# Kernel optimization log

Hardware: AMD Instinct MI355X
Metric: run time of the kernel (lower is better)

Reference implementation:

```python
import jax, jax.numpy as jnp
import numpy as np
from jax import lax

K, INC, OUC = 6, 64, 32
H, W = 512, 512
WIN = 128  # min(128, min(H,W)) for training path
ITERATION = 2  # torch uses random.randint(1,3); fixed for determinism


def setup_inputs() -> dict:
    key = jax.random.key(0)
    ks = jax.random.split(key, 12)
    s = 0.05
    return {
        "x": jax.random.uniform(ks[0], (K, 3, H, W), jnp.float32),
        "pred_list": jax.random.uniform(ks[1], (K, 3, H, W), jnp.float32),
        "feat_list": jax.random.normal(ks[2], (K, INC, H, W), jnp.float32) * 0.1,
        "split_w": jax.random.normal(ks[3], (3 * OUC, INC, 3, 3), jnp.float32) * s,
        "split_b": jax.random.normal(ks[4], (3 * OUC,), jnp.float32) * s,
        "merge1_w": jax.random.normal(ks[5], (INC, 3 * OUC + 3, 3, 3), jnp.float32) * s,
        "merge1_b": jax.random.normal(ks[6], (INC,), jnp.float32) * s,
        "merge2_w": jax.random.normal(ks[7], (INC, INC, 3, 3), jnp.float32) * s,
        "merge2_b": jax.random.normal(ks[8], (INC,), jnp.float32) * s,
        "head_w": jax.random.normal(ks[9], (3, INC, 3, 3), jnp.float32) * s,
        "head_b": jax.random.normal(ks[10], (3,), jnp.float32) * s,
    }


def _conv(x, w, b, groups=1):
    y = lax.conv_general_dilated(
        x, w, (1, 1), ((1, 1), (1, 1)),
        dimension_numbers=("NCHW", "OIHW", "NCHW"), feature_group_count=groups)
    return y + b[None, :, None, None]


def _get_box(pred_list):
    # B_cat = mean of bg channel, T_cat = sum of fg channel; distance map [H,W]
    B_cat = pred_list[:, 2].mean(axis=0)
    T_cat = pred_list[:, 0].sum(axis=0)
    distance = jnp.abs(1.0 - T_cat - B_cat)
    # nearest-neighbor downsample by 0.1: out[i,j] = in[10*i, 10*j]
    hs, ws = H // 10, W // 10
    ds = distance[::10, ::10][:hs, :ws]
    # NMS keep[0] (training path uses boxes[0:1]) == global argmax of score
    idx = jnp.argmax(ds.reshape(-1))
    cx = (idx % ws) * 10
    cy = (idx // ws) * 10
    half = WIN // 2
    x1, y1 = cx - half, cy - half
    x2, y2 = cx + half, cy + half
    ox = (-jnp.minimum(x1, 0) + jnp.minimum(W - x1, 0)
          - jnp.minimum(x2, 0) + jnp.minimum(W - x2, 0))
    oy = (-jnp.minimum(y1, 0) + jnp.minimum(H - y1, 0)
          - jnp.minimum(y2, 0) + jnp.minimum(H - y2, 0))
    return (y1 + oy).astype(jnp.int32), (x1 + ox).astype(jnp.int32)


def reference(x, pred_list, feat_list, split_w, split_b,
              merge1_w, merge1_b, merge2_w, merge2_b, head_w, head_b):
    c = INC
    y1, x1 = _get_box(pred_list)  # box fixed across iterations (computed once)
    x_patch = lax.dynamic_slice(x, (0, 0, y1, x1), (K, 3, WIN, WIN))
    feat_patch = lax.dynamic_slice(feat_list, (0, 0, y1, x1), (K, INC, WIN, WIN))
    feat_tiled = jnp.tile(feat_patch, (1, 3, 1, 1))
    denom = max(K - 1, 1)

    pl = pred_list
    for _ in range(ITERATION):
        pred_patch = lax.dynamic_slice(pl, (0, 0, y1, x1), (K, 3, WIN, WIN))
        # cat([p0.repeat(c), p1.repeat(c), p2.repeat(c)]) == repeat each channel c times
        attention = jnp.repeat(pred_patch, c, axis=1)
        fs = _conv(feat_tiled * attention, split_w, split_b, groups=3)
        f0, f1, f2 = fs[:, :OUC], fs[:, OUC:2 * OUC], fs[:, 2 * OUC:]
        feat_t = f1.sum(0, keepdims=True) / denom - f0.sum(0, keepdims=True) + 2.0 * f0
        feat_r = f0.sum(0, keepdims=True) - f0 + f1
        feat_b = jnp.broadcast_to(f2.mean(0, keepdims=True), f2.shape)
        fcat = jnp.concatenate([feat_t, feat_r, feat_b, x_patch], axis=1)
        h1 = jax.nn.leaky_relu(_conv(fcat, merge1_w, merge1_b), 0.2)
        fm = _conv(h1, merge2_w, merge2_b)
        pr = _conv(fm, head_w, head_b)
        inner = (jnp.tanh(pr[:, :, 10:WIN - 10, 10:WIN - 10]) + 1.0) / 2.0
        pl = lax.dynamic_update_slice(pl, inner, (0, 0, y1 + 10, x1 + 10))
    return pl
```

## Files before the change

### kernel.cpp

```cpp
#include <hip/hip_runtime.h>
#include <math.h>

typedef __attribute__((ext_vector_type(8))) short short8_t;
typedef __attribute__((ext_vector_type(4))) float f32x4;

#define Hh 512
#define Ww 512
#define IMG (Hh * Ww)
#define WINP 128
#define PP (WINP * WINP)

__device__ __forceinline__ unsigned short f2bf(float f) {
    unsigned int u = __builtin_bit_cast(unsigned int, f);
    u += 0x7fffu + ((u >> 16) & 1u);
    return (unsigned short)(u >> 16);
}
__device__ __forceinline__ float bf2f(unsigned short h) {
    unsigned int u = ((unsigned int)h) << 16;
    return __builtin_bit_cast(float, u);
}

__global__ void box_kernel(const float* __restrict__ pred, int* __restrict__ box) {
    int tid = threadIdx.x;
    float best = -1.0f; int bidx = 0x7fffffff;
    for (int cand = tid; cand < 51 * 51; cand += 256) {
        int i = cand / 51, j = cand % 51;
        int y = i * 10, x = j * 10;
        float T = 0.f, Bv = 0.f;
#pragma unroll
        for (int k = 0; k < 6; ++k) {
            T  += pred[((k * 3 + 0) * Hh + y) * Ww + x];
            Bv += pred[((k * 3 + 2) * Hh + y) * Ww + x];
        }
        float d = fabsf(1.0f - T - Bv / 6.0f);
        if (d > best || (d == best && cand < bidx)) { best = d; bidx = cand; }
    }
    __shared__ float sv[256];
    __shared__ int   si[256];
    sv[tid] = best; si[tid] = bidx;
    __syncthreads();
    for (int s = 128; s > 0; s >>= 1) {
        if (tid < s) {
            if (sv[tid + s] > sv[tid] || (sv[tid + s] == sv[tid] && si[tid + s] < si[tid])) {
                sv[tid] = sv[tid + s]; si[tid] = si[tid + s];
            }
        }
        __syncthreads();
    }
    if (tid == 0) {
        int idx = si[0];
        int cy = (idx / 51) * 10, cx = (idx % 51) * 10;
        int yy = cy - 64; yy = yy < 0 ? 0 : (yy > Hh - WINP ? Hh - WINP : yy);
        int xx = cx - 64; xx = xx < 0 ? 0 : (xx > Ww - WINP ? Ww - WINP : xx);
        box[0] = yy; box[1] = xx;
    }
}

__global__ void copy_kernel(const float4* __restrict__ src, float4* __restrict__ dst) {
    int i = blockIdx.x * 256 + threadIdx.x;
    dst[i] = src[i];
}

__global__ void prep_weights(const float* __restrict__ sw, const float* __restrict__ m1w,
                             const float* __restrict__ m2w, const float* __restrict__ hw,
                             unsigned short* __restrict__ WF)
{
    int idx = blockIdx.x * 256 + threadIdx.x;
    int j = idx & 7;
    int lane = (idx >> 3) & 63;
    int frag = idx >> 9;
    int n16 = lane & 15;
    int ko = (lane >> 4) * 8 + j;
    float v = 0.f;
    if (frag < 108) {
        int g = frag / 36; int r = frag % 36; int kc = r / 18; r %= 18; int tap = r / 2; int nf = r & 1;
        int oc = g * 32 + nf * 16 + n16; int ic = kc * 32 + ko;
        v = sw[(oc * 64 + ic) * 9 + tap];
    } else if (frag < 252) {
        int r = frag - 108; int half = r / 72; r %= 72; int kc = r / 18; r %= 18; int tap = r / 2; int nf = r & 1;
        int oc = half * 32 + nf * 16 + n16; int ic = kc * 32 + ko;
        if (ic < 99) v = m1w[(oc * 99 + ic) * 9 + tap];
    } else if (frag < 324) {
        int r = frag - 252; int half = r / 36; r %= 36; int kc = r / 18; r %= 18; int tap = r / 2; int nf = r & 1;
        int oc = half * 32 + nf * 16 + n16; int ic = kc * 32 + ko;
        v = m2w[(oc * 64 + ic) * 9 + tap];
    } else {
        int r = frag - 324; int kc = r / 9; int tap = r % 9;
        int ic = kc * 32 + ko;
        if (n16 < 3) v = hw[(n16 * 64 + ic) * 9 + tap];
    }
    WF[idx] = f2bf(v);
}

__global__ void prep_featcl(const float* __restrict__ feat, const int* __restrict__ box,
                            unsigned short* __restrict__ featcl)
{
    int row = blockIdx.x;
    int k = blockIdx.y;
    int t = threadIdx.x;
    int y1 = box[0], x1 = box[1];
    __shared__ unsigned short s[128 * 64];
    for (int i = 0; i < 32; ++i) {
        int idx = t + i * 256;
        int ic = idx >> 7, c = idx & 127;
        s[c * 64 + ic] = f2bf(feat[((size_t)(k * 64 + ic) * Hh + y1 + row) * Ww + x1 + c]);
    }
    __syncthreads();
    if (t < 128) {
        unsigned short* dst = &featcl[((size_t)k * 16384 + row * 128 + t) * 64];
        for (int i = 0; i < 8; ++i)
            *(short8_t*)&dst[i * 8] = *(short8_t*)&s[t * 64 + i * 8];
    }
}

__global__ __launch_bounds__(256) void split_mfma(
    const unsigned short* __restrict__ featcl, const float* __restrict__ pl,
    const unsigned short* __restrict__ WF, const float* __restrict__ sb,
    const int* __restrict__ box, unsigned short* __restrict__ fscl)
{
    const int tid = threadIdx.x;
    const int l = tid & 63, w = tid >> 6;
    const int T = blockIdx.x;
    const int k = blockIdx.y / 3, g = blockIdx.y % 3;
    const int ty0 = (T >> 3) * 16, tx0 = (T & 7) * 16;
    const int y1 = box[0], x1 = box[1];

    __shared__ __align__(16) unsigned short s_a[10368];
    __shared__ __align__(16) unsigned short s_b[9216];

    f32x4 acc[4][2];
#pragma unroll
    for (int mf = 0; mf < 4; ++mf)
#pragma unroll
        for (int nf = 0; nf < 2; ++nf) acc[mf][nf] = (f32x4){0.f, 0.f, 0.f, 0.f};

    const float* plg = pl + (size_t)(k * 3 + g) * IMG + (size_t)y1 * Ww + x1;
    const unsigned short* fck = featcl + (size_t)k * 16384 * 64;

    for (int kc = 0; kc < 2; ++kc) {
        __syncthreads();
#pragma unroll
        for (int i = 0; i < 6; ++i) {
            int s = tid + i * 256;
            if (s < 1296) {
                int pxs = s >> 2, q = s & 3;
                int r = pxs / 18, c = pxs - r * 18;
                int py = ty0 - 1 + r, px = tx0 - 1 + c;
                short8_t o;
                if (py >= 0 && py < WINP && px >= 0 && px < WINP) {
                    float pv = plg[py * Ww + px];
                    short8_t f = *(const short8_t*)&fck[(size_t)(py * WINP + px) * 64 + kc * 32 + q * 8];
#pragma unroll
                    for (int e = 0; e < 8; ++e) o[e] = (short)f2bf(bf2f((unsigned short)f[e]) * pv);
                } else {
#pragma unroll
                    for (int e = 0; e < 8; ++e) o[e] = 0;
                }
                *(short8_t*)&s_a[(r * 18 + c) * 32 + q * 8] = o;
            }
        }
        {
            const unsigned short* src = WF + (size_t)((g * 2 + kc) * 18) * 512;
#pragma unroll
            for (int i = 0; i < 5; ++i) {
                int cch = tid + i * 256;
                if (cch < 1152)
                    *(short8_t*)&s_b[cch * 8] = *(const short8_t*)&src[cch * 8];
            }
        }
        __syncthreads();
#pragma unroll
        for (int tap = 0; tap < 9; ++tap) {
            int dy = tap / 3, dx = tap % 3;
            short8_t a[4];
#pragma unroll
            for (int mf = 0; mf < 4; ++mf)
                a[mf] = *(const short8_t*)&s_a[((w * 4 + mf + dy) * 18 + (l & 15) + dx) * 32 + (l >> 4) * 8];
#pragma unroll
            for (int nf = 0; nf < 2; ++nf) {
                short8_t bfr = *(const short8_t*)&s_b[((tap * 2 + nf) * 64 + l) * 8];
#pragma unroll
                for (int mf = 0; mf < 4; ++mf)
                    acc[mf][nf] = __builtin_amdgcn_mfma_f32_16x16x32_bf16(a[mf], bfr, acc[mf][nf], 0, 0, 0);
            }
        }
    }
    __syncthreads();
    unsigned short* s_t = s_a;
#pragma unroll
    for (int nf = 0; nf < 2; ++nf) {
        float bias = sb[g * 32 + nf * 16 + (l & 15)];
#pragma unroll
        for (int mf = 0; mf < 4; ++mf) {
            int row = w * 4 + mf;
#pragma unroll
            for (int r = 0; r < 4; ++r) {
                int col = (l >> 4) * 4 + r;
                s_t[(row * 16 + col) * 32 + nf * 16 + (l & 15)] = f2bf(acc[mf][nf][r] + bias);
            }
        }
    }
    __syncthreads();
    {
        int row = tid >> 4, col = tid & 15;
        size_t gpx = (size_t)(ty0 + row) * WINP + tx0 + col;
        unsigned short* dst = fscl + ((size_t)k * 16384 + gpx) * 96 + g * 32;
#pragma unroll
        for (int i = 0; i < 4; ++i)
            *(short8_t*)&dst[i * 8] = *(short8_t*)&s_t[tid * 32 + i * 8];
    }
}

__global__ void reduce_kernel(const unsigned short* __restrict__ fscl, float* __restrict__ Scl)
{
    int tg = blockIdx.x * 256 + threadIdx.x;
    int px = tg >> 2, q = tg & 3;
    float s0[8], s1[8], s2[8];
#pragma unroll
    for (int e = 0; e < 8; ++e) { s0[e] = 0.f; s1[e] = 0.f; s2[e] = 0.f; }
#pragma unroll
    for (int k = 0; k < 6; ++k) {
        const unsigned short* p = &fscl[((size_t)k * 16384 + px) * 96 + q * 8];
        short8_t a0 = *(const short8_t*)&p[0];
        short8_t a1 = *(const short8_t*)&p[32];
        short8_t a2 = *(const short8_t*)&p[64];
#pragma unroll
        for (int e = 0; e < 8; ++e) {
            s0[e] += bf2f((unsigned short)a0[e]);
            s1[e] += bf2f((unsigned short)a1[e]);
            s2[e] += bf2f((unsigned short)a2[e]);
        }
    }
    float* d = &Scl[(size_t)px * 96 + q * 8];
#pragma unroll
    for (int e = 0; e < 8; ++e) {
        d[e]      = s1[e] * 0.2f - s0[e];
        d[32 + e] = s0[e];
        d[64 + e] = s2[e] * (1.f / 6.f);
    }
}

__global__ __launch_bounds__(256) void merge1_mfma(
    const unsigned short* __restrict__ fscl, const float* __restrict__ Scl,
    const float* __restrict__ x, const unsigned short* __restrict__ WF,
    const float* __restrict__ m1b, const int* __restrict__ box,
    unsigned short* __restrict__ h1cl)
{
    const int tid = threadIdx.x;
    const int l = tid & 63, w = tid >> 6;
    const int T = blockIdx.x;
    const int k = blockIdx.y >> 1, half = blockIdx.y & 1;
    const int ty0 = (T >> 3) * 16, tx0 = (T & 7) * 16;
    const int y1 = box[0], x1 = box[1];

    __shared__ __align__(16) unsigned short s_a[10368];
    __shared__ __align__(16) unsigned short s_b[9216];

    f32x4 acc[4][2];
#pragma unroll
    for (int mf = 0; mf < 4; ++mf)
#pragma unroll
        for (int nf = 0; nf < 2; ++nf) acc[mf][nf] = (f32x4){0.f, 0.f, 0.f, 0.f};

    for (int kc = 0; kc < 4; ++kc) {
        __syncthreads();
#pragma unroll
        for (int i = 0; i < 6; ++i) {
            int s = tid + i * 256;
            if (s < 1296) {
                int pxs = s >> 2, q = s & 3;
                int r = pxs / 18, c = pxs - r * 18;
                int py = ty0 - 1 + r, px = tx0 - 1 + c;
                short8_t o;
#pragma unroll
                for (int e = 0; e < 8; ++e) o[e] = 0;
                if (py >= 0 && py < WINP && px >= 0 && px < WINP) {
                    size_t gpx = (size_t)py * WINP + px;
                    if (kc == 0) {
                        short8_t f0 = *(const short8_t*)&fscl[((size_t)k * 16384 + gpx) * 96 + q * 8];
                        const float* S = &Scl[gpx * 96 + q * 8];
#pragma unroll
                        for (int e = 0; e < 8; ++e)
                            o[e] = (short)f2bf(S[e] + 2.f * bf2f((unsigned short)f0[e]));
                    } else if (kc == 1) {
                        const unsigned short* fp = &fscl[((size_t)k * 16384 + gpx) * 96];
                        short8_t f0 = *(const short8_t*)&fp[q * 8];
                        short8_t f1 = *(const short8_t*)&fp[32 + q * 8];
                        const float* S = &Scl[gpx * 96 + 32 + q * 8];
#pragma unroll
                        for (int e = 0; e < 8; ++e)
                            o[e] = (short)f2bf(S[e] - bf2f((unsigned short)f0[e]) + bf2f((unsigned short)f1[e]));
                    } else if (kc == 2) {
                        const float* S = &Scl[gpx * 96 + 64 + q * 8];
#pragma unroll
                        for (int e = 0; e < 8; ++e) o[e] = (short)f2bf(S[e]);
                    } else {
                        if (q == 0) {
#pragma unroll
                            for (int ch = 0; ch < 3; ++ch)
                                o[ch] = (short)f2bf(x[(size_t)(k * 3 + ch) * IMG + (size_t)(y1 + py) * Ww + x1 + px]);
                        }
                    }
                }
                *(short8_t*)&s_a[(r * 18 + c) * 32 + q * 8] = o;
            }
        }
        {
            const unsigned short* src = WF + (size_t)(108 + (half * 4 + kc) * 18) * 512;
#pragma unroll
            for (int i = 0; i < 5; ++i) {
                int cch = tid + i * 256;
                if (cch < 1152)
                    *(short8_t*)&s_b[cch * 8] = *(const short8_t*)&src[cch * 8];
            }
        }
        __syncthreads();
#pragma unroll
        for (int tap = 0; tap < 9; ++tap) {
            int dy = tap / 3, dx = tap % 3;
            short8_t a[4];
#pragma unroll
            for (int mf = 0; mf < 4; ++mf)
                a[mf] = *(const short8_t*)&s_a[((w * 4 + mf + dy) * 18 + (l & 15) + dx) * 32 + (l >> 4) * 8];
#pragma unroll
            for (int nf = 0; nf < 2; ++nf) {
                short8_t bfr = *(const short8_t*)&s_b[((tap * 2 + nf) * 64 + l) * 8];
#pragma unroll
                for (int mf = 0; mf < 4; ++mf)
                    acc[mf][nf] = __builtin_amdgcn_mfma_f32_16x16x32_bf16(a[mf], bfr, acc[mf][nf], 0, 0, 0);
            }
        }
    }
    __syncthreads();
    unsigned short* s_t = s_a;
#pragma unroll
    for (int nf = 0; nf < 2; ++nf) {
        float bias = m1b[half * 32 + nf * 16 + (l & 15)];
#pragma unroll
        for (int mf = 0; mf < 4; ++mf) {
            int row = w * 4 + mf;
#pragma unroll
            for (int r = 0; r < 4; ++r) {
                int col = (l >> 4) * 4 + r;
                float v = acc[mf][nf][r] + bias;
                v = v >= 0.f ? v : 0.2f * v;
                s_t[(row * 16 + col) * 32 + nf * 16 + (l & 15)] = f2bf(v);
            }
        }
    }
    __syncthreads();
    {
        int row = tid >> 4, col = tid & 15;
        size_t gpx = (size_t)(ty0 + row) * WINP + tx0 + col;
        unsigned short* dst = h1cl + ((size_t)k * 16384 + gpx) * 64 + half * 32;
#pragma unroll
        for (int i = 0; i < 4; ++i)
            *(short8_t*)&dst[i * 8] = *(short8_t*)&s_t[tid * 32 + i * 8];
    }
}

__global__ __launch_bounds__(256) void merge2_mfma(
    const unsigned short* __restrict__ h1cl, const unsigned short* __restrict__ WF,
    const float* __restrict__ m2b, unsigned short* __restrict__ h2cl)
{
    const int tid = threadIdx.x;
    const int l = tid & 63, w = tid >> 6;
    const int T = blockIdx.x;
    const int k = blockIdx.y >> 1, half = blockIdx.y & 1;
    const int ty0 = (T >> 3) * 16, tx0 = (T & 7) * 16;

    __shared__ __align__(16) unsigned short s_a[10368];
    __shared__ __align__(16) unsigned short s_b[9216];

    f32x4 acc[4][2];
#pragma unroll
    for (int mf = 0; mf < 4; ++mf)
#pragma unroll
        for (int nf = 0; nf < 2; ++nf) acc[mf][nf] = (f32x4){0.f, 0.f, 0.f, 0.f};

    const unsigned short* ink = h1cl + (size_t)k * 16384 * 64;

    for (int kc = 0; kc < 2; ++kc) {
        __syncthreads();
#pragma unroll
        for (int i = 0; i < 6; ++i) {
            int s = tid + i * 256;
            if (s < 1296) {
                int pxs = s >> 2, q = s & 3;
                int r = pxs / 18, c = pxs - r * 18;
                int py = ty0 - 1 + r, px = tx0 - 1 + c;
                short8_t o;
                if (py >= 0 && py < WINP && px >= 0 && px < WINP) {
                    o = *(const short8_t*)&ink[(size_t)(py * WINP + px) * 64 + kc * 32 + q * 8];
                } else {
#pragma unroll
                    for (int e = 0; e < 8; ++e) o[e] = 0;
                }
                *(short8_t*)&s_a[(r * 18 + c) * 32 + q * 8] = o;
            }
        }
        {
            const unsigned short* src = WF + (size_t)(252 + (half * 2 + kc) * 18) * 512;
#pragma unroll
            for (int i = 0; i < 5; ++i) {
                int cch = tid + i * 256;
                if (cch < 1152)
                    *(short8_t*)&s_b[cch * 8] = *(const short8_t*)&src[cch * 8];
            }
        }
        __syncthreads();
#pragma unroll
        for (int tap = 0; tap < 9; ++tap) {
            int dy = tap / 3, dx = tap % 3;
            short8_t a[4];
#pragma unroll
            for (int mf = 0; mf < 4; ++mf)
                a[mf] = *(const short8_t*)&s_a[((w * 4 + mf + dy) * 18 + (l & 15) + dx) * 32 + (l >> 4) * 8];
#pragma unroll
            for (int nf = 0; nf < 2; ++nf) {
                short8_t bfr = *(const short8_t*)&s_b[((tap * 2 + nf) * 64 + l) * 8];
#pragma unroll
                for (int mf = 0; mf < 4; ++mf)
                    acc[mf][nf] = __builtin_amdgcn_mfma_f32_16x16x32_bf16(a[mf], bfr, acc[mf][nf], 0, 0, 0);
            }
        }
    }
    __syncthreads();
    unsigned short* s_t = s_a;
#pragma unroll
    for (int nf = 0; nf < 2; ++nf) {
        float bias = m2b[half * 32 + nf * 16 + (l & 15)];
#pragma unroll
        for (int mf = 0; mf < 4; ++mf) {
            int row = w * 4 + mf;
#pragma unroll
            for (int r = 0; r < 4; ++r) {
                int col = (l >> 4) * 4 + r;
                s_t[(row * 16 + col) * 32 + nf * 16 + (l & 15)] = f2bf(acc[mf][nf][r] + bias);
            }
        }
    }
    __syncthreads();
    {
        int row = tid >> 4, col = tid & 15;
        size_t gpx = (size_t)(ty0 + row) * WINP + tx0 + col;
        unsigned short* dst = h2cl + ((size_t)k * 16384 + gpx) * 64 + half * 32;
#pragma unroll
        for (int i = 0; i < 4; ++i)
            *(short8_t*)&dst[i * 8] = *(short8_t*)&s_t[tid * 32 + i * 8];
    }
}

__global__ __launch_bounds__(256) void head_mfma(
    const unsigned short* __restrict__ h2cl, const unsigned short* __restrict__ WF,
    const float* __restrict__ hb, const int* __restrict__ box,
    float* __restrict__ out)
{
    const int tid = threadIdx.x;
    const int l = tid & 63, w = tid >> 6;
    const int T = blockIdx.x;
    const int k = blockIdx.y;
    const int oy0 = 10 + (T / 7) * 16, ox0 = 10 + (T % 7) * 16;
    const int y1 = box[0], x1 = box[1];

    __shared__ __align__(16) unsigned short s_a[10368];
    __shared__ __align__(16) unsigned short s_b[4608];

    f32x4 acc[4];
#pragma unroll
    for (int mf = 0; mf < 4; ++mf) acc[mf] = (f32x4){0.f, 0.f, 0.f, 0.f};

    const unsigned short* ink = h2cl + (size_t)k * 16384 * 64;

    for (int kc = 0; kc < 2; ++kc) {
        __syncthreads();
#pragma unroll
        for (int i = 0; i < 6; ++i) {
            int s = tid + i * 256;
            if (s < 1296) {
                int pxs = s >> 2, q = s & 3;
                int r = pxs / 18, c = pxs - r * 18;
                int py = oy0 - 1 + r, px = ox0 - 1 + c;
                *(short8_t*)&s_a[(r * 18 + c) * 32 + q * 8] =
                    *(const short8_t*)&ink[(size_t)(py * WINP + px) * 64 + kc * 32 + q * 8];
            }
        }
        {
            const unsigned short* src = WF + (size_t)(324 + kc * 9) * 512;
#pragma unroll
            for (int i = 0; i < 3; ++i) {
                int cch = tid + i * 256;
                if (cch < 576)
                    *(short8_t*)&s_b[cch * 8] = *(const short8_t*)&src[cch * 8];
            }
        }
        __syncthreads();
#pragma unroll
        for (int tap = 0; tap < 9; ++tap) {
            int dy = tap / 3, dx = tap % 3;
            short8_t bfr = *(const short8_t*)&s_b[(tap * 64 + l) * 8];
#pragma unroll
            for (int mf = 0; mf < 4; ++mf) {
                short8_t a = *(const short8_t*)&s_a[((w * 4 + mf + dy) * 18 + (l & 15) + dx) * 32 + (l >> 4) * 8];
                acc[mf] = __builtin_amdgcn_mfma_f32_16x16x32_bf16(a, bfr, acc[mf], 0, 0, 0);
            }
        }
    }
    int oc = l & 15;
    if (oc < 3) {
        float bias = hb[oc];
#pragma unroll
        for (int mf = 0; mf < 4; ++mf) {
            int row = oy0 + w * 4 + mf;
            if (row < 118) {
#pragma unroll
                for (int r = 0; r < 4; ++r) {
                    int col = ox0 + (l >> 4) * 4 + r;
                    if (col < 118) {
                        float v = (tanhf(acc[mf][r] + bias) + 1.0f) * 0.5f;
                        out[(size_t)(k * 3 + oc) * IMG + (size_t)(y1 + row) * Ww + x1 + col] = v;
                    }
                }
            }
        }
    }
}

extern "C" void kernel_launch(void* const* d_in, const int* in_sizes, int n_in,
                              void* d_out, int out_size, void* d_ws, size_t ws_size,
                              hipStream_t stream)
{
    const float* x       = (const float*)d_in[0];
    const float* pred    = (const float*)d_in[1];
    const float* feat    = (const float*)d_in[2];
    const float* split_w = (const float*)d_in[3];
    const float* split_b = (const float*)d_in[4];
    const float* m1w     = (const float*)d_in[5];
    const float* m1b     = (const float*)d_in[6];
    const float* m2w     = (const float*)d_in[7];
    const float* m2b     = (const float*)d_in[8];
    const float* hw      = (const float*)d_in[9];
    const float* hb      = (const float*)d_in[10];
    float* out = (float*)d_out;

    char* base = (char*)d_ws;
    size_t o = 0;
    int* box = (int*)(base + o);                  o += 256;
    unsigned short* WF = (unsigned short*)(base + o);      o += (size_t)175104 * 2;  o = (o + 255) & ~(size_t)255;
    unsigned short* featcl = (unsigned short*)(base + o);  o += (size_t)6 * 16384 * 64 * 2;
    unsigned short* fscl = (unsigned short*)(base + o);    o += (size_t)6 * 16384 * 96 * 2;
    float* Scl = (float*)(base + o);                       o += (size_t)16384 * 96 * 4;
    unsigned short* h1cl = (unsigned short*)(base + o);    o += (size_t)6 * 16384 * 64 * 2;
    unsigned short* h2cl = (unsigned short*)(base + o);    o += (size_t)6 * 16384 * 64 * 2;

    box_kernel<<<1, 256, 0, stream>>>(pred, box);
    prep_weights<<<684, 256, 0, stream>>>(split_w, m1w, m2w, hw, WF);
    prep_featcl<<<dim3(128, 6), 256, 0, stream>>>(feat, box, featcl);
    copy_kernel<<<4608, 256, 0, stream>>>((const float4*)pred, (float4*)out);

    for (int it = 0; it < 2; ++it) {
        split_mfma<<<dim3(64, 18), 256, 0, stream>>>(featcl, out, WF, split_b, box, fscl);
        reduce_kernel<<<256, 256, 0, stream>>>(fscl, Scl);
        merge1_mfma<<<dim3(64, 12), 256, 0, stream>>>(fscl, Scl, x, WF, m1b, box, h1cl);
        merge2_mfma<<<dim3(64, 12), 256, 0, stream>>>(h1cl, WF, m2b, h2cl);
        head_mfma<<<dim3(49, 6), 256, 0, stream>>>(h2cl, WF, hb, box, out);
    }
}
```

Before: 695.6 us.

## Read conv weights directly from global, reorder LDS layout, merge output-channel halves

All four conv kernels stop staging weights in shared memory and read the B fragments straight from global (L1/L2-cached) memory. The A-tile LDS layout changes from pixel-major to quarter-channel-major, which spreads lanes across banks. merge1 and merge2 now compute all 64 output channels per block instead of splitting them into halves, so the halo input tile is staged once. The cost is half as many blocks, more accumulator registers, and weight loads exposed to global latency inside the MFMA loop.

Result: slower. 805.3 us (+15.8%).

```diff
diff --git a/kernel.cpp b/kernel.cpp
--- a/kernel.cpp
+++ b/kernel.cpp
@@ -126,7 +126,6 @@
     const int y1 = box[0], x1 = box[1];
 
     __shared__ __align__(16) unsigned short s_a[10368];
-    __shared__ __align__(16) unsigned short s_b[9216];
 
     f32x4 acc[4][2];
 #pragma unroll
@@ -156,29 +155,21 @@
 #pragma unroll
                     for (int e = 0; e < 8; ++e) o[e] = 0;
                 }
-                *(short8_t*)&s_a[(r * 18 + c) * 32 + q * 8] = o;
-            }
-        }
-        {
-            const unsigned short* src = WF + (size_t)((g * 2 + kc) * 18) * 512;
-#pragma unroll
-            for (int i = 0; i < 5; ++i) {
-                int cch = tid + i * 256;
-                if (cch < 1152)
-                    *(short8_t*)&s_b[cch * 8] = *(const short8_t*)&src[cch * 8];
-            }
-        }
-        __syncthreads();
+                *(short8_t*)&s_a[(q * 324 + pxs) * 8] = o;
+            }
+        }
+        __syncthreads();
+        const unsigned short* Bp = WF + ((size_t)(g * 2 + kc) * 18) * 512 + (size_t)l * 8;
 #pragma unroll
         for (int tap = 0; tap < 9; ++tap) {
             int dy = tap / 3, dx = tap % 3;
             short8_t a[4];
 #pragma unroll
             for (int mf = 0; mf < 4; ++mf)
-                a[mf] = *(const short8_t*)&s_a[((w * 4 + mf + dy) * 18 + (l & 15) + dx) * 32 + (l >> 4) * 8];
+                a[mf] = *(const short8_t*)&s_a[((l >> 4) * 324 + (w * 4 + mf + dy) * 18 + (l & 15) + dx) * 8];
 #pragma unroll
             for (int nf = 0; nf < 2; ++nf) {
-                short8_t bfr = *(const short8_t*)&s_b[((tap * 2 + nf) * 64 + l) * 8];
+                short8_t bfr = *(const short8_t*)&Bp[(size_t)(tap * 2 + nf) * 512];
 #pragma unroll
                 for (int mf = 0; mf < 4; ++mf)
                     acc[mf][nf] = __builtin_amdgcn_mfma_f32_16x16x32_bf16(a[mf], bfr, acc[mf][nf], 0, 0, 0);
@@ -190,13 +181,14 @@
 #pragma unroll
     for (int nf = 0; nf < 2; ++nf) {
         float bias = sb[g * 32 + nf * 16 + (l & 15)];
+        int slot = nf * 2 + ((l & 15) >> 3);
 #pragma unroll
         for (int mf = 0; mf < 4; ++mf) {
             int row = w * 4 + mf;
 #pragma unroll
             for (int r = 0; r < 4; ++r) {
                 int col = (l >> 4) * 4 + r;
-                s_t[(row * 16 + col) * 32 + nf * 16 + (l & 15)] = f2bf(acc[mf][nf][r] + bias);
+                s_t[(slot * 256 + row * 16 + col) * 8 + (l & 7)] = f2bf(acc[mf][nf][r] + bias);
             }
         }
     }
@@ -207,7 +199,7 @@
         unsigned short* dst = fscl + ((size_t)k * 16384 + gpx) * 96 + g * 32;
 #pragma unroll
         for (int i = 0; i < 4; ++i)
-            *(short8_t*)&dst[i * 8] = *(short8_t*)&s_t[tid * 32 + i * 8];
+            *(short8_t*)&dst[i * 8] = *(short8_t*)&s_t[(i * 256 + tid) * 8];
     }
 }
 
@@ -249,18 +241,17 @@
     const int tid = threadIdx.x;
     const int l = tid & 63, w = tid >> 6;
     const int T = blockIdx.x;
-    const int k = blockIdx.y >> 1, half = blockIdx.y & 1;
+    const int k = blockIdx.y;
     const int ty0 = (T >> 3) * 16, tx0 = (T & 7) * 16;
     const int y1 = box[0], x1 = box[1];
 
     __shared__ __align__(16) unsigned short s_a[10368];
-    __shared__ __align__(16) unsigned short s_b[9216];
-
-    f32x4 acc[4][2];
+
+    f32x4 acc[4][4];
 #pragma unroll
     for (int mf = 0; mf < 4; ++mf)
 #pragma unroll
-        for (int nf = 0; nf < 2; ++nf) acc[mf][nf] = (f32x4){0.f, 0.f, 0.f, 0.f};
+        for (int n = 0; n < 4; ++n) acc[mf][n] = (f32x4){0.f, 0.f, 0.f, 0.f};
 
     for (int kc = 0; kc < 4; ++kc) {
         __syncthreads();
@@ -302,60 +293,59 @@
                         }
                     }
                 }
-                *(short8_t*)&s_a[(r * 18 + c) * 32 + q * 8] = o;
-            }
-        }
-        {
-            const unsigned short* src = WF + (size_t)(108 + (half * 4 + kc) * 18) * 512;
-#pragma unroll
-            for (int i = 0; i < 5; ++i) {
-                int cch = tid + i * 256;
-                if (cch < 1152)
-                    *(short8_t*)&s_b[cch * 8] = *(const short8_t*)&src[cch * 8];
-            }
-        }
-        __syncthreads();
+                *(short8_t*)&s_a[(q * 324 + pxs) * 8] = o;
+            }
+        }
+        __syncthreads();
+        const unsigned short* Bp = WF + ((size_t)(108 + kc * 18)) * 512 + (size_t)l * 8;
 #pragma unroll
         for (int tap = 0; tap < 9; ++tap) {
             int dy = tap / 3, dx = tap % 3;
             short8_t a[4];
 #pragma unroll
             for (int mf = 0; mf < 4; ++mf)
-                a[mf] = *(const short8_t*)&s_a[((w * 4 + mf + dy) * 18 + (l & 15) + dx) * 32 + (l >> 4) * 8];
-#pragma unroll
-            for (int nf = 0; nf < 2; ++nf) {
-                short8_t bfr = *(const short8_t*)&s_b[((tap * 2 + nf) * 64 + l) * 8];
+                a[mf] = *(const short8_t*)&s_a[((l >> 4) * 324 + (w * 4 + mf + dy) * 18 + (l & 15) + dx) * 8];
+#pragma unroll
+            for (int n = 0; n < 4; ++n) {
+                int half = n >> 1, nf2 = n & 1;
+                short8_t bfr = *(const short8_t*)&Bp[((size_t)half * 72 + tap * 2 + nf2) * 512];
 #pragma unroll
                 for (int mf = 0; mf < 4; ++mf)
-                    acc[mf][nf] = __builtin_amdgcn_mfma_f32_16x16x32_bf16(a[mf], bfr, acc[mf][nf], 0, 0, 0);
+                    acc[mf][n] = __builtin_amdgcn_mfma_f32_16x16x32_bf16(a[mf], bfr, acc[mf][n], 0, 0, 0);
             }
         }
     }
     __syncthreads();
     unsigned short* s_t = s_a;
 #pragma unroll
-    for (int nf = 0; nf < 2; ++nf) {
-        float bias = m1b[half * 32 + nf * 16 + (l & 15)];
-#pragma unroll
-        for (int mf = 0; mf < 4; ++mf) {
-            int row = w * 4 + mf;
-#pragma unroll
-            for (int r = 0; r < 4; ++r) {
-                int col = (l >> 4) * 4 + r;
-                float v = acc[mf][nf][r] + bias;
-                v = v >= 0.f ? v : 0.2f * v;
-                s_t[(row * 16 + col) * 32 + nf * 16 + (l & 15)] = f2bf(v);
-            }
-        }
-    }
-    __syncthreads();
-    {
-        int row = tid >> 4, col = tid & 15;
-        size_t gpx = (size_t)(ty0 + row) * WINP + tx0 + col;
-        unsigned short* dst = h1cl + ((size_t)k * 16384 + gpx) * 64 + half * 32;
-#pragma unroll
-        for (int i = 0; i < 4; ++i)
-            *(short8_t*)&dst[i * 8] = *(short8_t*)&s_t[tid * 32 + i * 8];
+    for (int h = 0; h < 2; ++h) {
+#pragma unroll
+        for (int nf2 = 0; nf2 < 2; ++nf2) {
+            int n = h * 2 + nf2;
+            float bias = m1b[n * 16 + (l & 15)];
+            int slot = nf2 * 2 + ((l & 15) >> 3);
+#pragma unroll
+            for (int mf = 0; mf < 4; ++mf) {
+                int row = w * 4 + mf;
+#pragma unroll
+                for (int r = 0; r < 4; ++r) {
+                    int col = (l >> 4) * 4 + r;
+                    float v = acc[mf][n][r] + bias;
+                    v = v >= 0.f ? v : 0.2f * v;
+                    s_t[(slot * 256 + row * 16 + col) * 8 + (l & 7)] = f2bf(v);
+                }
+            }
+        }
+        __syncthreads();
+        {
+            int row = tid >> 4, col = tid & 15;
+            size_t gpx = (size_t)(ty0 + row) * WINP + tx0 + col;
+            unsigned short* dst = h1cl + ((size_t)k * 16384 + gpx) * 64 + h * 32;
+#pragma unroll
+            for (int i = 0; i < 4; ++i)
+                *(short8_t*)&dst[i * 8] = *(short8_t*)&s_t[(i * 256 + tid) * 8];
+        }
+        __syncthreads();
     }
 }
 
@@ -366,17 +356,16 @@
     const int tid = threadIdx.x;
     const int l = tid & 63, w = tid >> 6;
     const int T = blockIdx.x;
-    const int k = blockIdx.y >> 1, half = blockIdx.y & 1;
+    const int k = blockIdx.y;
     const int ty0 = (T >> 3) * 16, tx0 = (T & 7) * 16;
 
     __shared__ __align__(16) unsigned short s_a[10368];
-    __shared__ __align__(16) unsigned short s_b[9216];
-
-    f32x4 acc[4][2];
+
+    f32x4 acc[4][4];
 #pragma unroll
     for (int mf = 0; mf < 4; ++mf)
 #pragma unroll
-        for (int nf = 0; nf < 2; ++nf) acc[mf][nf] = (f32x4){0.f, 0.f, 0.f, 0.f};
+        for (int n = 0; n < 4; ++n) acc[mf][n] = (f32x4){0.f, 0.f, 0.f, 0.f};
 
     const unsigned short* ink = h1cl + (size_t)k * 16384 * 64;
 
@@ -396,58 +385,57 @@
 #pragma unroll
                     for (int e = 0; e < 8; ++e) o[e] = 0;
                 }
-                *(short8_t*)&s_a[(r * 18 + c) * 32 + q * 8] = o;
-            }
-        }
-        {
-            const unsigned short* src = WF + (size_t)(252 + (half * 2 + kc) * 18) * 512;
-#pragma unroll
-            for (int i = 0; i < 5; ++i) {
-                int cch = tid + i * 256;
-                if (cch < 1152)
-                    *(short8_t*)&s_b[cch * 8] = *(const short8_t*)&src[cch * 8];
-            }
-        }
-        __syncthreads();
+                *(short8_t*)&s_a[(q * 324 + pxs) * 8] = o;
+            }
+        }
+        __syncthreads();
+        const unsigned short* Bp = WF + ((size_t)(252 + kc * 18)) * 512 + (size_t)l * 8;
 #pragma unroll
         for (int tap = 0; tap < 9; ++tap) {
             int dy = tap / 3, dx = tap % 3;
             short8_t a[4];
 #pragma unroll
             for (int mf = 0; mf < 4; ++mf)
-                a[mf] = *(const short8_t*)&s_a[((w * 4 + mf + dy) * 18 + (l & 15) + dx) * 32 + (l >> 4) * 8];
-#pragma unroll
-            for (int nf = 0; nf < 2; ++nf) {
-                short8_t bfr = *(const short8_t*)&s_b[((tap * 2 + nf) * 64 + l) * 8];
+                a[mf] = *(const short8_t*)&s_a[((l >> 4) * 324 + (w * 4 + mf + dy) * 18 + (l & 15) + dx) * 8];
+#pragma unroll
+            for (int n = 0; n < 4; ++n) {
+                int half = n >> 1, nf2 = n & 1;
+                short8_t bfr = *(const short8_t*)&Bp[((size_t)half * 36 + tap * 2 + nf2) * 512];
 #pragma unroll
                 for (int mf = 0; mf < 4; ++mf)
-                    acc[mf][nf] = __builtin_amdgcn_mfma_f32_16x16x32_bf16(a[mf], bfr, acc[mf][nf], 0, 0, 0);
+                    acc[mf][n] = __builtin_amdgcn_mfma_f32_16x16x32_bf16(a[mf], bfr, acc[mf][n], 0, 0, 0);
             }
         }
     }
     __syncthreads();
     unsigned short* s_t = s_a;
 #pragma unroll
-    for (int nf = 0; nf < 2; ++nf) {
-        float bias = m2b[half * 32 + nf * 16 + (l & 15)];
-#pragma unroll
-        for (int mf = 0; mf < 4; ++mf) {
-            int row = w * 4 + mf;
-#pragma unroll
-            for (int r = 0; r < 4; ++r) {
-                int col = (l >> 4) * 4 + r;
-                s_t[(row * 16 + col) * 32 + nf * 16 + (l & 15)] = f2bf(acc[mf][nf][r] + bias);
-            }
-        }
-    }
-    __syncthreads();
-    {
-        int row = tid >> 4, col = tid & 15;
-        size_t gpx = (size_t)(ty0 + row) * WINP + tx0 + col;
-        unsigned short* dst = h2cl + ((size_t)k * 16384 + gpx) * 64 + half * 32;
-#pragma unroll
-        for (int i = 0; i < 4; ++i)
-            *(short8_t*)&dst[i * 8] = *(short8_t*)&s_t[tid * 32 + i * 8];
+    for (int h = 0; h < 2; ++h) {
+#pragma unroll
+        for (int nf2 = 0; nf2 < 2; ++nf2) {
+            int n = h * 2 + nf2;
+            float bias = m2b[n * 16 + (l & 15)];
+            int slot = nf2 * 2 + ((l & 15) >> 3);
+#pragma unroll
+            for (int mf = 0; mf < 4; ++mf) {
+                int row = w * 4 + mf;
+#pragma unroll
+                for (int r = 0; r < 4; ++r) {
+                    int col = (l >> 4) * 4 + r;
+                    s_t[(slot * 256 + row * 16 + col) * 8 + (l & 7)] = f2bf(acc[mf][n][r] + bias);
+                }
+            }
+        }
+        __syncthreads();
+        {
+            int row = tid >> 4, col = tid & 15;
+            size_t gpx = (size_t)(ty0 + row) * WINP + tx0 + col;
+            unsigned short* dst = h2cl + ((size_t)k * 16384 + gpx) * 64 + h * 32;
+#pragma unroll
+            for (int i = 0; i < 4; ++i)
+                *(short8_t*)&dst[i * 8] = *(short8_t*)&s_t[(i * 256 + tid) * 8];
+        }
+        __syncthreads();
     }
 }
 
@@ -464,7 +452,6 @@
     const int y1 = box[0], x1 = box[1];
 
     __shared__ __align__(16) unsigned short s_a[10368];
-    __shared__ __align__(16) unsigned short s_b[4608];
 
     f32x4 acc[4];
 #pragma unroll
@@ -481,27 +468,19 @@
                 int pxs = s >> 2, q = s & 3;
                 int r = pxs / 18, c = pxs - r * 18;
                 int py = oy0 - 1 + r, px = ox0 - 1 + c;
-                *(short8_t*)&s_a[(r * 18 + c) * 32 + q * 8] =
+                *(short8_t*)&s_a[(q * 324 + pxs) * 8] =
                     *(const short8_t*)&ink[(size_t)(py * WINP + px) * 64 + kc * 32 + q * 8];
             }
         }
-        {
-            const unsigned short* src = WF + (size_t)(324 + kc * 9) * 512;
-#pragma unroll
-            for (int i = 0; i < 3; ++i) {
-                int cch = tid + i * 256;
-                if (cch < 576)
-                    *(short8_t*)&s_b[cch * 8] = *(const short8_t*)&src[cch * 8];
-            }
-        }
-        __syncthreads();
+        __syncthreads();
+        const unsigned short* Bp = WF + ((size_t)(324 + kc * 9)) * 512 + (size_t)l * 8;
 #pragma unroll
         for (int tap = 0; tap < 9; ++tap) {
             int dy = tap / 3, dx = tap % 3;
-            short8_t bfr = *(const short8_t*)&s_b[(tap * 64 + l) * 8];
+            short8_t bfr = *(const short8_t*)&Bp[(size_t)tap * 512];
 #pragma unroll
             for (int mf = 0; mf < 4; ++mf) {
-                short8_t a = *(const short8_t*)&s_a[((w * 4 + mf + dy) * 18 + (l & 15) + dx) * 32 + (l >> 4) * 8];
+                short8_t a = *(const short8_t*)&s_a[((l >> 4) * 324 + (w * 4 + mf + dy) * 18 + (l & 15) + dx) * 8];
                 acc[mf] = __builtin_amdgcn_mfma_f32_16x16x32_bf16(a, bfr, acc[mf], 0, 0, 0);
             }
         }
@@ -561,8 +540,8 @@
     for (int it = 0; it < 2; ++it) {
         split_mfma<<<dim3(64, 18), 256, 0, stream>>>(featcl, out, WF, split_b, box, fscl);
         reduce_kernel<<<256, 256, 0, stream>>>(fscl, Scl);
-        merge1_mfma<<<dim3(64, 12), 256, 0, stream>>>(fscl, Scl, x, WF, m1b, box, h1cl);
-        merge2_mfma<<<dim3(64, 12), 256, 0, stream>>>(h1cl, WF, m2b, h2cl);
+        merge1_mfma<<<dim3(64, 6), 256, 0, stream>>>(fscl, Scl, x, WF, m1b, box, h1cl);
+        merge2_mfma<<<dim3(64, 6), 256, 0, stream>>>(h1cl, WF, m2b, h2cl);
         head_mfma<<<dim3(49, 6), 256, 0, stream>>>(h2cl, WF, hb, box, out);
     }
 }
```
